# Kernel tuning notes

Measured on AMD Instinct MI355X. Metric: run time of the kernel, lower is better.

The kernel has to match this reference:

```python
import jax, jax.numpy as jnp
import numpy as np

B, N, E, H = 4, 2048, 1024, 16
D = E // H
SCALE = 1.0 / np.sqrt(D).astype(np.float32)


def setup_inputs() -> dict:
    key = jax.random.key(0)
    ks = jax.random.split(key, 8)
    xq = jax.random.normal(ks[0], (B, N, E), jnp.float32)
    xk = jax.random.normal(ks[1], (B, N, E), jnp.float32)
    xv = jax.random.normal(ks[2], (B, N, E), jnp.float32)
    # causal mask: True means 'masked out' (matches masked_fill_ semantics)
    attn_mask = jnp.triu(jnp.ones((N, N), dtype=bool), k=1)[None, None]
    Wq = jax.random.normal(ks[3], (E, E), jnp.float32) / np.sqrt(E)
    Wk = jax.random.normal(ks[4], (E, E), jnp.float32) / np.sqrt(E)
    Wv = jax.random.normal(ks[5], (E, E), jnp.float32) / np.sqrt(E)
    Wo = jax.random.normal(ks[6], (E, E), jnp.float32) / np.sqrt(E)
    bo = jnp.zeros((E,), jnp.float32)
    return {"xq": xq, "xk": xk, "xv": xv, "attn_mask": attn_mask,
            "Wq": Wq, "Wk": Wk, "Wv": Wv, "Wo": Wo, "bo": bo}


def _split_heads(x):
    # [B, N, E] -> [B, H, N, D]
    return x.reshape(B, N, H, D).transpose(0, 2, 1, 3)


def reference(xq, xk, xv, attn_mask, Wq, Wk, Wv, Wo, bo):
    # torch nn.Linear: y = x @ W.T
    q = _split_heads(xq @ Wq.T)
    k = _split_heads(xk @ Wk.T)
    v = _split_heads(xv @ Wv.T)
    scores = SCALE * jnp.einsum('bhqd,bhkd->bhqk', q, k)
    scores = jnp.where(attn_mask, -jnp.inf, scores)
    attn = jax.nn.softmax(scores, axis=-1)
    out = jnp.einsum('bhqk,bhkd->bhqd', attn, v)
    out = out.transpose(0, 2, 1, 3).reshape(B, N, E)  # merge heads
    return out @ Wo.T + bo
```

## Files before the change

kernel.cpp:

```cpp
#include <hip/hip_runtime.h>
#include <hip/hip_bf16.h>
#include <stdint.h>
#include <stddef.h>

#define B_ 4
#define N_ 2048
#define E_ 1024
#define H_ 16
#define D_ 64

using bf16 = __hip_bfloat16;
typedef __bf16 bf16x8 __attribute__((ext_vector_type(8)));
typedef float  f32x4  __attribute__((ext_vector_type(4)));

__device__ inline bf16x8 load8(const float* p) {
    f32x4 a = *(const f32x4*)p;
    f32x4 b = *(const f32x4*)(p + 4);
    bf16x8 r;
#pragma unroll
    for (int e = 0; e < 4; e++) { r[e] = (__bf16)a[e]; r[e + 4] = (__bf16)b[e]; }
    return r;
}
__device__ inline void store_elem(float* C, size_t idx, float v) { C[idx] = v; }
__device__ inline void store_elem(bf16* C, size_t idx, float v) {
    C[idx] = __float2bfloat16(v);
}

__device__ inline void async_stage16(const bf16* g, bf16* l) {
    __builtin_amdgcn_global_load_lds(
        (const __attribute__((address_space(1))) uint32_t*)g,
        (__attribute__((address_space(3))) uint32_t*)l, 16, 0, 0);
}
__device__ inline void manual_stage16(const float* g, bf16* l) {
    *(bf16x8*)l = load8(g);
}

__global__ __launch_bounds__(256) void cvt_all(
    const float* __restrict__ w0, const float* __restrict__ w1,
    const float* __restrict__ w2, const float* __restrict__ w3,
    bf16* __restrict__ wd,
    const float* __restrict__ x0, const float* __restrict__ x1,
    const float* __restrict__ x2,
    bf16* __restrict__ xd0, bf16* __restrict__ xd1, bf16* __restrict__ xd2)
{
    int bx = blockIdx.x;
    const float* s; bf16* d;
    if (bx < 2048) {
        const int seg = bx >> 9;
        s = seg == 0 ? w0 : seg == 1 ? w1 : seg == 2 ? w2 : w3;
        d = wd + (size_t)seg * (E_ * E_);
        bx &= 511;
    } else {
        bx -= 2048;
        const int seg = bx >> 12;
        s = seg == 0 ? x0 : seg == 1 ? x1 : x2;
        d = seg == 0 ? xd0 : seg == 1 ? xd1 : xd2;
        bx &= 4095;
    }
    const size_t off = ((size_t)bx * 256 + threadIdx.x) * 8;
    *(bf16x8*)&d[off] = load8(s + off);
}

struct GemmB { const void* A[3]; void* C[3]; };

template <typename TA, typename TC>
__global__ __launch_bounds__(256) void gemm_bt(
    GemmB batch, const bf16* __restrict__ Wb, const float* __restrict__ bias)
{
    __shared__ bf16 As[128 * 32];
    __shared__ bf16 Bs[128 * 32];

    const TA*   __restrict__ A = (const TA*)batch.A[blockIdx.z];
    TC*         __restrict__ C = (TC*)batch.C[blockIdx.z];
    const bf16* __restrict__ W = Wb + (size_t)blockIdx.z * (E_ * E_);

    const int tid  = threadIdx.x;
    const int lane = tid & 63;
    const int wave = tid >> 6;
    const int wr   = wave >> 1;
    const int wc   = wave & 1;
    const int r    = lane & 15;
    const int quad = lane >> 4;

    const int m0 = blockIdx.y * 128;
    const int n0 = blockIdx.x * 128;

    const int row0 = tid >> 2,         cc0 = (tid & 3) * 8;
    const int row1 = (tid + 256) >> 2, cc1 = cc0;

    f32x4 acc[4][4];
#pragma unroll
    for (int i = 0; i < 4; i++)
#pragma unroll
        for (int j = 0; j < 4; j++)
            acc[i][j] = {0.0f, 0.0f, 0.0f, 0.0f};

    for (int k0 = 0; k0 < E_; k0 += 32) {
        __syncthreads();
        if constexpr (__is_same(TA, bf16)) {
            async_stage16(&A[(size_t)(m0 + row0) * E_ + k0 + cc0], &As[tid * 8]);
            async_stage16(&A[(size_t)(m0 + row1) * E_ + k0 + cc1], &As[(tid + 256) * 8]);
        } else {
            manual_stage16(&A[(size_t)(m0 + row0) * E_ + k0 + cc0], &As[tid * 8]);
            manual_stage16(&A[(size_t)(m0 + row1) * E_ + k0 + cc1], &As[(tid + 256) * 8]);
        }
        async_stage16(&W[(size_t)(n0 + row0) * E_ + k0 + cc0], &Bs[tid * 8]);
        async_stage16(&W[(size_t)(n0 + row1) * E_ + k0 + cc1], &Bs[(tid + 256) * 8]);
        __syncthreads();

        bf16x8 a[4], b[4];
#pragma unroll
        for (int mt = 0; mt < 4; mt++)
            a[mt] = *(const bf16x8*)&As[(wr * 64 + mt * 16 + r) * 32 + quad * 8];
#pragma unroll
        for (int nt = 0; nt < 4; nt++)
            b[nt] = *(const bf16x8*)&Bs[(wc * 64 + nt * 16 + r) * 32 + quad * 8];
#pragma unroll
        for (int mt = 0; mt < 4; mt++)
#pragma unroll
            for (int nt = 0; nt < 4; nt++)
                acc[mt][nt] = __builtin_amdgcn_mfma_f32_16x16x32_bf16(
                    a[mt], b[nt], acc[mt][nt], 0, 0, 0);
    }

#pragma unroll
    for (int mt = 0; mt < 4; mt++) {
#pragma unroll
        for (int nt = 0; nt < 4; nt++) {
            const int col = n0 + wc * 64 + nt * 16 + r;
            float bv = bias ? bias[col] : 0.0f;
#pragma unroll
            for (int rg = 0; rg < 4; rg++) {
                const int row = m0 + wr * 64 + mt * 16 + quad * 4 + rg;
                store_elem(C, (size_t)row * E_ + col, acc[mt][nt][rg] + bv);
            }
        }
    }
}

__global__ __launch_bounds__(256) void attn_fwd(
    const bf16* __restrict__ q, const bf16* __restrict__ k,
    const bf16* __restrict__ v, bf16* __restrict__ o)
{
    constexpr int LS = 72;
    __shared__ bf16 Ks[2][64 * LS];
    __shared__ bf16 Vt[2][64 * LS];
    __shared__ bf16 Ps[128 * LS];

    const int tid  = threadIdx.x;
    const int lane = tid & 63;
    const int wave = tid >> 6;
    const int r    = lane & 15;
    const int quad = lane >> 4;

    const int bh = blockIdx.y;
    const int b  = bh >> 4;
    const int h  = bh & 15;
    const int p  = blockIdx.x;

    const size_t basek = (size_t)b * N_ * E_ + (size_t)h * D_;

    const int key0 = tid >> 3;
    const int key1 = key0 + 32;
    const int ck   = (tid & 7) * 8;
    const int kp   = tid & 31;
    const int cv   = (tid >> 5) * 8;

#pragma unroll
    for (int ph = 0; ph < 2; ph++) {
        const int xb = ph == 0 ? (15 - p) : p;
        const int q0 = xb * 128;
        const int nt = 2 * xb + 2;

        bf16x8 qB[2][2];
#pragma unroll
        for (int s = 0; s < 2; s++) {
            const size_t qrow =
                ((size_t)b * N_ + q0 + wave * 32 + s * 16 + r) * E_ + h * D_;
            qB[s][0] = *(const bf16x8*)&q[qrow + quad * 8];
            qB[s][1] = *(const bf16x8*)&q[qrow + quad * 8 + 32];
#pragma unroll
            for (int ks = 0; ks < 2; ks++)
#pragma unroll
                for (int e = 0; e < 8; e++)
                    qB[s][ks][e] = (__bf16)((float)qB[s][ks][e] * 0.125f);
        }

        float m_i[2] = {-1e30f, -1e30f};
        float l_i[2] = {0.0f, 0.0f};
        f32x4 o_acc[4][2];
#pragma unroll
        for (int dt = 0; dt < 4; dt++)
#pragma unroll
            for (int s = 0; s < 2; s++)
                o_acc[dt][s] = {0.0f, 0.0f, 0.0f, 0.0f};

        bf16x8 kp0, kp1, vp0, vp1;
        kp0 = *(const bf16x8*)&k[basek + (size_t)key0 * E_ + ck];
        kp1 = *(const bf16x8*)&k[basek + (size_t)key1 * E_ + ck];
        vp0 = *(const bf16x8*)&v[basek + (size_t)(2 * kp) * E_ + cv];
        vp1 = *(const bf16x8*)&v[basek + (size_t)(2 * kp + 1) * E_ + cv];
        *(bf16x8*)&Ks[0][key0 * LS + ck] = kp0;
        *(bf16x8*)&Ks[0][key1 * LS + ck] = kp1;
#pragma unroll
        for (int e = 0; e < 8; e++) {
            union { __bf16 hh[2]; uint32_t u; } pk;
            pk.hh[0] = vp0[e]; pk.hh[1] = vp1[e];
            *(uint32_t*)&Vt[0][(cv + e) * LS + 2 * kp] = pk.u;
        }
        {
            const size_t j1 = 64;
            kp0 = *(const bf16x8*)&k[basek + (j1 + key0) * E_ + ck];
            kp1 = *(const bf16x8*)&k[basek + (j1 + key1) * E_ + ck];
            vp0 = *(const bf16x8*)&v[basek + (j1 + 2 * kp) * E_ + cv];
            vp1 = *(const bf16x8*)&v[basek + (j1 + 2 * kp + 1) * E_ + cv];
        }
        __syncthreads();

        for (int t = 0; t < nt; t++) {
            const int cur = t & 1;

            if (t + 1 < nt) {
                *(bf16x8*)&Ks[cur ^ 1][key0 * LS + ck] = kp0;
                *(bf16x8*)&Ks[cur ^ 1][key1 * LS + ck] = kp1;
#pragma unroll
                for (int e = 0; e < 8; e++) {
                    union { __bf16 hh[2]; uint32_t u; } pk;
                    pk.hh[0] = vp0[e]; pk.hh[1] = vp1[e];
                    *(uint32_t*)&Vt[cur ^ 1][(cv + e) * LS + 2 * kp] = pk.u;
                }
            }
            if (t + 2 < nt) {
                const size_t j2 = (size_t)(t + 2) * 64;
                kp0 = *(const bf16x8*)&k[basek + (j2 + key0) * E_ + ck];
                kp1 = *(const bf16x8*)&k[basek + (j2 + key1) * E_ + ck];
                vp0 = *(const bf16x8*)&v[basek + (j2 + 2 * kp) * E_ + cv];
                vp1 = *(const bf16x8*)&v[basek + (j2 + 2 * kp + 1) * E_ + cv];
            }

            f32x4 sf[4][2];
#pragma unroll
            for (int mt = 0; mt < 4; mt++)
#pragma unroll
                for (int s = 0; s < 2; s++)
                    sf[mt][s] = {0.0f, 0.0f, 0.0f, 0.0f};
#pragma unroll
            for (int ks = 0; ks < 2; ks++)
#pragma unroll
                for (int mt = 0; mt < 4; mt++) {
                    bf16x8 ka = *(const bf16x8*)
                        &Ks[cur][(mt * 16 + r) * LS + ks * 32 + quad * 8];
#pragma unroll
                    for (int s = 0; s < 2; s++)
                        sf[mt][s] = __builtin_amdgcn_mfma_f32_16x16x32_bf16(
                            ka, qB[s][ks], sf[mt][s], 0, 0, 0);
                }

            if (t >= nt - 2) {
#pragma unroll
                for (int mt = 0; mt < 4; mt++)
#pragma unroll
                    for (int s = 0; s < 2; s++) {
                        const int qgl = q0 + wave * 32 + s * 16 + r;
#pragma unroll
                        for (int rg = 0; rg < 4; rg++) {
                            const int kgl = t * 64 + mt * 16 + quad * 4 + rg;
                            if (kgl > qgl) sf[mt][s][rg] = -1e30f;
                        }
                    }
            }

#pragma unroll
            for (int s = 0; s < 2; s++) {
                float mx = sf[0][s][0];
#pragma unroll
                for (int mt = 0; mt < 4; mt++)
#pragma unroll
                    for (int rg = 0; rg < 4; rg++)
                        mx = fmaxf(mx, sf[mt][s][rg]);
                mx = fmaxf(mx, __shfl_xor(mx, 16));
                mx = fmaxf(mx, __shfl_xor(mx, 32));
                const float m_new = fmaxf(m_i[s], mx);
                const float al = __expf(m_i[s] - m_new);
                m_i[s] = m_new;

                float ls = 0.0f;
                const int prow = (wave * 32 + s * 16 + r) * LS;
#pragma unroll
                for (int mt = 0; mt < 4; mt++) {
                    const float p0 = __expf(sf[mt][s][0] - m_new);
                    const float p1 = __expf(sf[mt][s][1] - m_new);
                    const float p2 = __expf(sf[mt][s][2] - m_new);
                    const float p3 = __expf(sf[mt][s][3] - m_new);
                    ls += (p0 + p1) + (p2 + p3);
                    union { __bf16 hh[4]; uint2 u2; } pk;
                    pk.hh[0] = (__bf16)p0; pk.hh[1] = (__bf16)p1;
                    pk.hh[2] = (__bf16)p2; pk.hh[3] = (__bf16)p3;
                    *(uint2*)&Ps[prow + mt * 16 + quad * 4] = pk.u2;
                }
                ls += __shfl_xor(ls, 16);
                ls += __shfl_xor(ls, 32);
                l_i[s] = l_i[s] * al + ls;
#pragma unroll
                for (int dt = 0; dt < 4; dt++)
#pragma unroll
                    for (int rg = 0; rg < 4; rg++)
                        o_acc[dt][s][rg] *= al;
            }

#pragma unroll
            for (int ks = 0; ks < 2; ks++) {
                bf16x8 pb[2];
#pragma unroll
                for (int s = 0; s < 2; s++)
                    pb[s] = *(const bf16x8*)
                        &Ps[(wave * 32 + s * 16 + r) * LS + ks * 32 + quad * 8];
#pragma unroll
                for (int dt = 0; dt < 4; dt++) {
                    bf16x8 va = *(const bf16x8*)
                        &Vt[cur][(dt * 16 + r) * LS + ks * 32 + quad * 8];
#pragma unroll
                    for (int s = 0; s < 2; s++)
                        o_acc[dt][s] = __builtin_amdgcn_mfma_f32_16x16x32_bf16(
                            va, pb[s], o_acc[dt][s], 0, 0, 0);
                }
            }

            __syncthreads();
        }

#pragma unroll
        for (int s = 0; s < 2; s++) {
            const float invl = 1.0f / l_i[s];
            const size_t orow =
                ((size_t)b * N_ + q0 + wave * 32 + s * 16 + r) * E_ + h * D_;
#pragma unroll
            for (int dt = 0; dt < 4; dt++) {
                union { __bf16 hh[4]; uint2 u2; } pk;
#pragma unroll
                for (int rg = 0; rg < 4; rg++)
                    pk.hh[rg] = (__bf16)(o_acc[dt][s][rg] * invl);
                *(uint2*)&o[orow + dt * 16 + quad * 4] = pk.u2;
            }
        }
    }
}

extern "C" void kernel_launch(void* const* d_in, const int* in_sizes, int n_in,
                              void* d_out, int out_size, void* d_ws, size_t ws_size,
                              hipStream_t stream) {
    const float* xq = (const float*)d_in[0];
    const float* xk = (const float*)d_in[1];
    const float* xv = (const float*)d_in[2];
    const float* Wq = (const float*)d_in[4];
    const float* Wk = (const float*)d_in[5];
    const float* Wv = (const float*)d_in[6];
    const float* Wo = (const float*)d_in[7];
    const float* bo = (const float*)d_in[8];
    float* out = (float*)d_out;

    const size_t elems = (size_t)B_ * N_ * E_;
    const size_t wel   = (size_t)E_ * E_;
    bf16* q   = (bf16*)d_ws;
    bf16* kk  = q + elems;
    bf16* vv  = kk + elems;
    bf16* ao  = vv + elems;
    bf16* Wb  = ao + elems;
    bf16* xb0 = Wb + 4 * wel;
    bf16* xb1 = xb0 + elems;
    bf16* xb2 = xb1 + elems;

    const size_t need_big = (7 * elems + 4 * wel) * 2;
    const bool big = ws_size >= need_big;

    dim3 blk(256);
    if (big) {
        cvt_all<<<dim3(14336), blk, 0, stream>>>(
            Wq, Wk, Wv, Wo, Wb, xq, xk, xv, xb0, xb1, xb2);
    } else {
        cvt_all<<<dim3(2048), blk, 0, stream>>>(
            Wq, Wk, Wv, Wo, Wb, nullptr, nullptr, nullptr,
            nullptr, nullptr, nullptr);
    }

    GemmB proj;
    if (big) { proj.A[0] = xb0; proj.A[1] = xb1; proj.A[2] = xb2; }
    else     { proj.A[0] = xq;  proj.A[1] = xk;  proj.A[2] = xv;  }
    proj.C[0] = q; proj.C[1] = kk; proj.C[2] = vv;
    if (big)
        gemm_bt<bf16, bf16><<<dim3(E_ / 128, (B_ * N_) / 128, 3), blk, 0, stream>>>(
            proj, Wb, nullptr);
    else
        gemm_bt<float, bf16><<<dim3(E_ / 128, (B_ * N_) / 128, 3), blk, 0, stream>>>(
            proj, Wb, nullptr);

    attn_fwd<<<dim3(8, B_ * H_), blk, 0, stream>>>(q, kk, vv, ao);

    GemmB fin;
    fin.A[0] = ao; fin.A[1] = ao; fin.A[2] = ao;
    fin.C[0] = out; fin.C[1] = out; fin.C[2] = out;
    gemm_bt<bf16, float><<<dim3(E_ / 128, (B_ * N_) / 128, 1), blk, 0, stream>>>(
        fin, Wb + 3 * wel, bo);
}
```

Before: 340.5 us.

## Switch attention to 32x32x16 MFMA with register-resident P via permlane32 swap

```diff
diff --git a/kernel.cpp b/kernel.cpp
--- a/kernel.cpp
+++ b/kernel.cpp
@@ -12,6 +12,8 @@
 using bf16 = __hip_bfloat16;
 typedef __bf16 bf16x8 __attribute__((ext_vector_type(8)));
 typedef float  f32x4  __attribute__((ext_vector_type(4)));
+typedef float  f32x16 __attribute__((ext_vector_type(16)));
+typedef unsigned int u32x2 __attribute__((ext_vector_type(2)));
 
 __device__ inline bf16x8 load8(const float* p) {
     f32x4 a = *(const f32x4*)p;
@@ -143,15 +145,15 @@
     const bf16* __restrict__ v, bf16* __restrict__ o)
 {
     constexpr int LS = 72;
+    constexpr float LOG2E = 1.44269504088896340736f;
     __shared__ bf16 Ks[2][64 * LS];
     __shared__ bf16 Vt[2][64 * LS];
-    __shared__ bf16 Ps[128 * LS];
 
     const int tid  = threadIdx.x;
     const int lane = tid & 63;
     const int wave = tid >> 6;
-    const int r    = lane & 15;
-    const int quad = lane >> 4;
+    const int l31  = lane & 31;
+    const int hi   = lane >> 5;
 
     const int bh = blockIdx.y;
     const int b  = bh >> 4;
@@ -172,28 +174,24 @@
         const int q0 = xb * 128;
         const int nt = 2 * xb + 2;
 
-        bf16x8 qB[2][2];
-#pragma unroll
-        for (int s = 0; s < 2; s++) {
-            const size_t qrow =
-                ((size_t)b * N_ + q0 + wave * 32 + s * 16 + r) * E_ + h * D_;
-            qB[s][0] = *(const bf16x8*)&q[qrow + quad * 8];
-            qB[s][1] = *(const bf16x8*)&q[qrow + quad * 8 + 32];
-#pragma unroll
-            for (int ks = 0; ks < 2; ks++)
+        bf16x8 qB[4];
+        {
+            const size_t qoff =
+                ((size_t)b * N_ + q0 + wave * 32 + l31) * E_ + h * D_ + hi * 8;
+#pragma unroll
+            for (int kc = 0; kc < 4; kc++) {
+                qB[kc] = *(const bf16x8*)&q[qoff + kc * 16];
 #pragma unroll
                 for (int e = 0; e < 8; e++)
-                    qB[s][ks][e] = (__bf16)((float)qB[s][ks][e] * 0.125f);
-        }
-
-        float m_i[2] = {-1e30f, -1e30f};
-        float l_i[2] = {0.0f, 0.0f};
-        f32x4 o_acc[4][2];
-#pragma unroll
-        for (int dt = 0; dt < 4; dt++)
-#pragma unroll
-            for (int s = 0; s < 2; s++)
-                o_acc[dt][s] = {0.0f, 0.0f, 0.0f, 0.0f};
+                    qB[kc][e] = (__bf16)((float)qB[kc][e] * 0.125f);
+            }
+        }
+
+        float m_i = -1e30f;
+        float l_i = 0.0f;
+        f32x16 o_acc[2];
+#pragma unroll
+        for (int rg = 0; rg < 16; rg++) { o_acc[0][rg] = 0.0f; o_acc[1][rg] = 0.0f; }
 
         bf16x8 kp0, kp1, vp0, vp1;
         kp0 = *(const bf16x8*)&k[basek + (size_t)key0 * E_ + ck];
@@ -238,110 +236,116 @@
                 vp1 = *(const bf16x8*)&v[basek + (j2 + 2 * kp + 1) * E_ + cv];
             }
 
-            f32x4 sf[4][2];
-#pragma unroll
-            for (int mt = 0; mt < 4; mt++)
-#pragma unroll
-                for (int s = 0; s < 2; s++)
-                    sf[mt][s] = {0.0f, 0.0f, 0.0f, 0.0f};
-#pragma unroll
-            for (int ks = 0; ks < 2; ks++)
-#pragma unroll
-                for (int mt = 0; mt < 4; mt++) {
-                    bf16x8 ka = *(const bf16x8*)
-                        &Ks[cur][(mt * 16 + r) * LS + ks * 32 + quad * 8];
-#pragma unroll
-                    for (int s = 0; s < 2; s++)
-                        sf[mt][s] = __builtin_amdgcn_mfma_f32_16x16x32_bf16(
-                            ka, qB[s][ks], sf[mt][s], 0, 0, 0);
+            f32x16 sf[2];
+#pragma unroll
+            for (int rg = 0; rg < 16; rg++) { sf[0][rg] = 0.0f; sf[1][rg] = 0.0f; }
+#pragma unroll
+            for (int kc = 0; kc < 4; kc++) {
+                bf16x8 ka0 = *(const bf16x8*)&Ks[cur][l31 * LS + kc * 16 + hi * 8];
+                bf16x8 ka1 = *(const bf16x8*)&Ks[cur][(32 + l31) * LS + kc * 16 + hi * 8];
+                sf[0] = __builtin_amdgcn_mfma_f32_32x32x16_bf16(ka0, qB[kc], sf[0], 0, 0, 0);
+                sf[1] = __builtin_amdgcn_mfma_f32_32x32x16_bf16(ka1, qB[kc], sf[1], 0, 0, 0);
+            }
+
+            if (t >= nt - 2) {
+                const int qgl   = q0 + wave * 32 + l31;
+                const int kbase = t * 64 + 4 * hi;
+#pragma unroll
+                for (int mt = 0; mt < 2; mt++)
+#pragma unroll
+                    for (int rg = 0; rg < 16; rg++) {
+                        const int kgl = kbase + mt * 32 + (rg & 3) + 8 * (rg >> 2);
+                        if (kgl > qgl) sf[mt][rg] = -1e30f;
+                    }
+            }
+
+            float mhalf[8];
+#pragma unroll
+            for (int i = 0; i < 8; i++)
+                mhalf[i] = fmaxf(fmaxf(sf[0][2 * i], sf[0][2 * i + 1]),
+                                 fmaxf(sf[1][2 * i], sf[1][2 * i + 1]));
+            float mx = fmaxf(fmaxf(fmaxf(mhalf[0], mhalf[1]), fmaxf(mhalf[2], mhalf[3])),
+                             fmaxf(fmaxf(mhalf[4], mhalf[5]), fmaxf(mhalf[6], mhalf[7])));
+            mx = fmaxf(mx, __shfl_xor(mx, 32));
+
+            if (!__all(mx <= m_i + 8.0f)) {
+                const float m_new = fmaxf(m_i, mx);
+                const float al = exp2f((m_i - m_new) * LOG2E);
+                l_i *= al;
+#pragma unroll
+                for (int mo = 0; mo < 2; mo++)
+#pragma unroll
+                    for (int rg = 0; rg < 16; rg++) o_acc[mo][rg] *= al;
+                m_i = m_new;
+            }
+
+            const float m2 = m_i * LOG2E;
+#pragma unroll
+            for (int mt = 0; mt < 2; mt++)
+#pragma unroll
+                for (int rg = 0; rg < 16; rg++)
+                    sf[mt][rg] = exp2f(__builtin_fmaf(sf[mt][rg], LOG2E, -m2));
+
+            float ls = 0.0f;
+#pragma unroll
+            for (int mt = 0; mt < 2; mt++) {
+                const float a0 = (sf[mt][0] + sf[mt][1]) + (sf[mt][2] + sf[mt][3]);
+                const float a1 = (sf[mt][4] + sf[mt][5]) + (sf[mt][6] + sf[mt][7]);
+                const float a2 = (sf[mt][8] + sf[mt][9]) + (sf[mt][10] + sf[mt][11]);
+                const float a3 = (sf[mt][12] + sf[mt][13]) + (sf[mt][14] + sf[mt][15]);
+                ls += (a0 + a1) + (a2 + a3);
+            }
+            ls += __shfl_xor(ls, 32);
+            l_i += ls;
+
+            uint32_t w[2][8];
+#pragma unroll
+            for (int mt = 0; mt < 2; mt++)
+#pragma unroll
+                for (int i = 0; i < 8; i++) {
+                    union { __bf16 hh[2]; uint32_t u; } pk;
+                    pk.hh[0] = (__bf16)sf[mt][2 * i];
+                    pk.hh[1] = (__bf16)sf[mt][2 * i + 1];
+                    w[mt][i] = pk.u;
                 }
 
-            if (t >= nt - 2) {
-#pragma unroll
-                for (int mt = 0; mt < 4; mt++)
-#pragma unroll
-                    for (int s = 0; s < 2; s++) {
-                        const int qgl = q0 + wave * 32 + s * 16 + r;
-#pragma unroll
-                        for (int rg = 0; rg < 4; rg++) {
-                            const int kgl = t * 64 + mt * 16 + quad * 4 + rg;
-                            if (kgl > qgl) sf[mt][s][rg] = -1e30f;
-                        }
-                    }
-            }
-
-#pragma unroll
-            for (int s = 0; s < 2; s++) {
-                float mx = sf[0][s][0];
-#pragma unroll
-                for (int mt = 0; mt < 4; mt++)
-#pragma unroll
-                    for (int rg = 0; rg < 4; rg++)
-                        mx = fmaxf(mx, sf[mt][s][rg]);
-                mx = fmaxf(mx, __shfl_xor(mx, 16));
-                mx = fmaxf(mx, __shfl_xor(mx, 32));
-                const float m_new = fmaxf(m_i[s], mx);
-                const float al = __expf(m_i[s] - m_new);
-                m_i[s] = m_new;
-
-                float ls = 0.0f;
-                const int prow = (wave * 32 + s * 16 + r) * LS;
-#pragma unroll
-                for (int mt = 0; mt < 4; mt++) {
-                    const float p0 = __expf(sf[mt][s][0] - m_new);
-                    const float p1 = __expf(sf[mt][s][1] - m_new);
-                    const float p2 = __expf(sf[mt][s][2] - m_new);
-                    const float p3 = __expf(sf[mt][s][3] - m_new);
-                    ls += (p0 + p1) + (p2 + p3);
+#pragma unroll
+            for (int ks = 0; ks < 4; ks++) {
+                const int c  = 4 * (ks & 1);
+                const int mt = ks >> 1;
+                u32x2 r1 = __builtin_amdgcn_permlane32_swap(
+                    w[mt][c + 0], w[mt][c + 2], false, false);
+                u32x2 r2 = __builtin_amdgcn_permlane32_swap(
+                    w[mt][c + 1], w[mt][c + 3], false, false);
+                union { uint32_t u[4]; bf16x8 v8; } pbu;
+                pbu.u[0] = r1[0]; pbu.u[1] = r2[0];
+                pbu.u[2] = r1[1]; pbu.u[3] = r2[1];
+#pragma unroll
+                for (int mo = 0; mo < 2; mo++) {
+                    bf16x8 va = *(const bf16x8*)
+                        &Vt[cur][(mo * 32 + l31) * LS + ks * 16 + hi * 8];
+                    o_acc[mo] = __builtin_amdgcn_mfma_f32_32x32x16_bf16(
+                        va, pbu.v8, o_acc[mo], 0, 0, 0);
+                }
+            }
+
+            __syncthreads();
+        }
+
+        {
+            const float invl = 1.0f / l_i;
+            const size_t orow =
+                ((size_t)b * N_ + q0 + wave * 32 + l31) * E_ + h * D_;
+#pragma unroll
+            for (int mo = 0; mo < 2; mo++)
+#pragma unroll
+                for (int g = 0; g < 4; g++) {
                     union { __bf16 hh[4]; uint2 u2; } pk;
-                    pk.hh[0] = (__bf16)p0; pk.hh[1] = (__bf16)p1;
-                    pk.hh[2] = (__bf16)p2; pk.hh[3] = (__bf16)p3;
-                    *(uint2*)&Ps[prow + mt * 16 + quad * 4] = pk.u2;
+#pragma unroll
+                    for (int j = 0; j < 4; j++)
+                        pk.hh[j] = (__bf16)(o_acc[mo][4 * g + j] * invl);
+                    *(uint2*)&o[orow + mo * 32 + 8 * g + 4 * hi] = pk.u2;
                 }
-                ls += __shfl_xor(ls, 16);
-                ls += __shfl_xor(ls, 32);
-                l_i[s] = l_i[s] * al + ls;
-#pragma unroll
-                for (int dt = 0; dt < 4; dt++)
-#pragma unroll
-                    for (int rg = 0; rg < 4; rg++)
-                        o_acc[dt][s][rg] *= al;
-            }
-
-#pragma unroll
-            for (int ks = 0; ks < 2; ks++) {
-                bf16x8 pb[2];
-#pragma unroll
-                for (int s = 0; s < 2; s++)
-                    pb[s] = *(const bf16x8*)
-                        &Ps[(wave * 32 + s * 16 + r) * LS + ks * 32 + quad * 8];
-#pragma unroll
-                for (int dt = 0; dt < 4; dt++) {
-                    bf16x8 va = *(const bf16x8*)
-                        &Vt[cur][(dt * 16 + r) * LS + ks * 32 + quad * 8];
-#pragma unroll
-                    for (int s = 0; s < 2; s++)
-                        o_acc[dt][s] = __builtin_amdgcn_mfma_f32_16x16x32_bf16(
-                            va, pb[s], o_acc[dt][s], 0, 0, 0);
-                }
-            }
-
-            __syncthreads();
-        }
-
-#pragma unroll
-        for (int s = 0; s < 2; s++) {
-            const float invl = 1.0f / l_i[s];
-            const size_t orow =
-                ((size_t)b * N_ + q0 + wave * 32 + s * 16 + r) * E_ + h * D_;
-#pragma unroll
-            for (int dt = 0; dt < 4; dt++) {
-                union { __bf16 hh[4]; uint2 u2; } pk;
-#pragma unroll
-                for (int rg = 0; rg < 4; rg++)
-                    pk.hh[rg] = (__bf16)(o_acc[dt][s][rg] * invl);
-                *(uint2*)&o[orow + dt * 16 + quad * 4] = pk.u2;
-            }
         }
     }
 }
```

After: 353.9 us. 3.9% more time.
